# Kernel tuning notes

Hardware: AMD Instinct MI355X
Metric: run time of the kernel (lower is better)

The kernel has to match this reference:

```python
import jax, jax.numpy as jnp
import numpy as np

N_NODES = 50000
N_EDGES = 800000
IN_C, HID_C, OUT_C = 128, 128, 1


def setup_inputs() -> dict:
    key = jax.random.key(0)
    ks = jax.random.split(key, 10)
    x = jax.random.normal(ks[0], (N_NODES, IN_C), dtype=jnp.float32)
    x2 = jax.random.normal(ks[1], (1,), dtype=jnp.float32)
    edge_index = jax.random.randint(ks[2], (2, N_EDGES), 0, N_NODES, dtype=jnp.int64)
    # GCNConv params (glorot-ish scale) and final linear
    W1 = jax.random.normal(ks[3], (IN_C, HID_C), dtype=jnp.float32) / np.sqrt(IN_C)
    b1 = jnp.zeros((HID_C,), dtype=jnp.float32)
    W2 = jax.random.normal(ks[4], (HID_C, HID_C), dtype=jnp.float32) / np.sqrt(HID_C)
    b2 = jnp.zeros((HID_C,), dtype=jnp.float32)
    Wlin = jax.random.normal(ks[5], (HID_C, OUT_C), dtype=jnp.float32) / np.sqrt(HID_C)
    blin = jnp.zeros((OUT_C,), dtype=jnp.float32)
    return {"x": x, "x2": x2, "edge_index": edge_index, "num_nodes": N_NODES,
            "W1": W1, "b1": b1, "W2": W2, "b2": b2, "Wlin": Wlin, "blin": blin}


def _gcn_conv(h, W, b, src, dst, norm, num_nodes):
    # linear transform then normalized scatter-add aggregation (PyG GCNConv)
    h = h @ W  # [N, C_out]
    msg = h[src] * norm[:, None]  # gather + scale, [E+N, C_out]
    out = jax.ops.segment_sum(msg, dst, num_segments=num_nodes)
    return out + b


def _gcn_norm(edge_index, num_nodes):
    # add self-loops, compute sym-normalization coefficients D^-1/2 A D^-1/2
    loop = jnp.arange(num_nodes, dtype=edge_index.dtype)
    src = jnp.concatenate([edge_index[0], loop])
    dst = jnp.concatenate([edge_index[1], loop])
    ones = jnp.ones(src.shape[0], dtype=jnp.float32)
    deg = jax.ops.segment_sum(ones, dst, num_segments=num_nodes)
    dinv = jnp.where(deg > 0, jax.lax.rsqrt(deg), 0.0)
    norm = dinv[src] * dinv[dst]
    return src, dst, norm


def reference(x, x2, edge_index, num_nodes, W1, b1, W2, b2, Wlin, blin):
    src, dst, norm = _gcn_norm(edge_index, num_nodes)
    h = _gcn_conv(x, W1, b1, src, dst, norm, num_nodes)
    h = jax.nn.relu(h)
    # dropout is identity in eval mode
    h = _gcn_conv(h, W2, b2, src, dst, norm, num_nodes)
    h = jax.nn.relu(h)
    out = h @ Wlin + blin  # [N, 1]
    return out.squeeze(-1)
```

## Files before the change

### kernel.cpp

```cpp
#include <hip/hip_runtime.h>
#include <hip/hip_bf16.h>

#define N_NODES 50000
#define N_EDGES 800000
#define C 128

#define NBB   391
#define CAPB  2600
#define CHUNK 2048

typedef __attribute__((ext_vector_type(8))) short short8v;
typedef __attribute__((ext_vector_type(4))) float f32x4;

__device__ __forceinline__ unsigned int bf16rtn(float f) {
    unsigned int u = __float_as_uint(f);
    return (u + 0x7fffu + ((u >> 16) & 1u)) >> 16;
}
__device__ __forceinline__ unsigned int packbf2(float lo, float hi) {
    return bf16rtn(lo) | (bf16rtn(hi) << 16);
}

__global__ void k_prepW(const float* __restrict__ W1, const float* __restrict__ W2,
                        unsigned short* __restrict__ Wsplit, int* __restrict__ gcur) {
    int t = blockIdx.x * 256 + threadIdx.x;
    if (t < NBB) gcur[t] = 0;
    if (t >= 32768) return;
    int layer = t >> 14, idx = t & 16383;
    int i = idx >> 7, j = idx & 127;
    const float* Wsrc = layer ? W2 : W1;
    float w = Wsrc[i * 128 + j];
    unsigned int h = bf16rtn(w);
    float hf = __uint_as_float(h << 16);
    unsigned int l = bf16rtn(w - hf);
    unsigned short* base = Wsplit + layer * 32768;
    base[j * 128 + i] = (unsigned short)h;
    base[16384 + j * 128 + i] = (unsigned short)l;
}

__global__ __launch_bounds__(256) void k_binA(const int* __restrict__ ei,
                                              int* __restrict__ gcur,
                                              int2* __restrict__ tmp) {
    __shared__ int hist[NBB];
    __shared__ int lbase[NBB];
    __shared__ int gbaseL[NBB];
    __shared__ int wsum[4];
    __shared__ int2 buf[CHUNK];
    __shared__ int totalv;

    int tid = threadIdx.x;
    int e0 = blockIdx.x * CHUNK;

    for (int i = tid; i < NBB; i += 256) hist[i] = 0;
    __syncthreads();

    int sarr[8], darr[8], parr[8];
#pragma unroll
    for (int j = 0; j < 8; ++j) {
        int e = e0 + j * 256 + tid;
        darr[j] = -1;
        if (e < N_EDGES) {
            sarr[j] = ei[e];
            int d = ei[N_EDGES + e];
            darr[j] = d;
            parr[j] = atomicAdd(&hist[d >> 7], 1);
        }
    }
    __syncthreads();

    {
        int i0 = 2 * tid, i1 = i0 + 1;
        int c0 = (i0 < NBB) ? hist[i0] : 0;
        int c1 = (i1 < NBB) ? hist[i1] : 0;
        int c = c0 + c1;
        int lane = tid & 63, w = tid >> 6;
        int s = c;
#pragma unroll
        for (int d = 1; d < 64; d <<= 1) {
            int u = __shfl_up(s, d, 64);
            if (lane >= d) s += u;
        }
        if (lane == 63) wsum[w] = s;
        __syncthreads();
        int add = 0;
        for (int i = 0; i < w; ++i) add += wsum[i];
        int incl = s + add;
        int excl = incl - c;
        if (i0 < NBB) lbase[i0] = excl;
        if (i1 < NBB) lbase[i1] = excl + c0;
        if (tid == 255) totalv = incl;
    }
    for (int i = tid; i < NBB; i += 256) {
        int cnt = hist[i];
        int run = (cnt > 0) ? atomicAdd(&gcur[i], cnt) : 0;
        gbaseL[i] = i * CAPB + run;
    }
    __syncthreads();

#pragma unroll
    for (int j = 0; j < 8; ++j) {
        if (darr[j] >= 0) {
            int b = darr[j] >> 7;
            buf[lbase[b] + parr[j]] = make_int2(sarr[j], darr[j]);
        }
    }
    __syncthreads();

    int total = totalv;
    for (int i = tid; i < total; i += 256) {
        int2 v = buf[i];
        int b = v.y >> 7;
        int gpos = gbaseL[b] + (i - lbase[b]);
        if (gpos < (b + 1) * CAPB) tmp[gpos] = v;
    }
}

__global__ __launch_bounds__(256) void k_dinv(const int2* __restrict__ tmp,
                                              const int* __restrict__ gcur,
                                              float* __restrict__ dinv) {
    __shared__ int cnt[128];
    int b = blockIdx.x, tid = threadIdx.x;
    if (tid < 128) cnt[tid] = 0;
    __syncthreads();
    int n = gcur[b];
    if (n > CAPB) n = CAPB;
    for (int i = tid; i < n; i += 256)
        atomicAdd(&cnt[tmp[b * CAPB + i].y & 127], 1);
    __syncthreads();
    int node = b * 128 + tid;
    if (tid < 128 && node < N_NODES)
        dinv[node] = rsqrtf((float)cnt[tid] + 1.0f);
}

template <bool AF32>
__global__ __launch_bounds__(512, 4) void k_gemm(const void* __restrict__ Ain,
                                                 const unsigned short* __restrict__ Whg,
                                                 const unsigned short* __restrict__ Wlg,
                                                 const float* __restrict__ dinv,
                                                 unsigned short* __restrict__ Hout) {
    __shared__ uint4 Al[64 * 16];
    __shared__ float ddv[64];

    int tid = threadIdx.x;
    int row0 = blockIdx.x * 64;
    int wv = tid >> 6, lane = tid & 63;
    int col = wv * 16 + (lane & 15);
    int kq = lane >> 4;

    const uint4* Bh4 = (const uint4*)Whg;
    const uint4* Bl4 = (const uint4*)Wlg;
    short8v bh[4], bl[4];
#pragma unroll
    for (int ks = 0; ks < 4; ++ks) {
        uint4 uh = Bh4[col * 16 + ks * 4 + kq];
        uint4 ul = Bl4[col * 16 + ks * 4 + kq];
        bh[ks] = *reinterpret_cast<short8v*>(&uh);
        bl[ks] = *reinterpret_cast<short8v*>(&ul);
    }

#pragma unroll
    for (int pass = 0; pass < 2; ++pass) {
        int row = (tid >> 4) + pass * 32;
        int o = tid & 15;
        int gr = row0 + row;
        uint4 u = make_uint4(0u, 0u, 0u, 0u);
        if (AF32) {
            float4 v0 = make_float4(0.f, 0.f, 0.f, 0.f), v1 = v0;
            if (gr < N_NODES) {
                const float4* A4 = (const float4*)Ain;
                v0 = A4[gr * 32 + o * 2];
                v1 = A4[gr * 32 + o * 2 + 1];
            }
            u.x = packbf2(v0.x, v0.y);
            u.y = packbf2(v0.z, v0.w);
            u.z = packbf2(v1.x, v1.y);
            u.w = packbf2(v1.z, v1.w);
        } else {
            if (gr < N_NODES) u = ((const uint4*)Ain)[gr * 16 + o];
        }
        int byte = (row * 256 + o * 16) ^ ((row & 7) << 4);
        Al[byte >> 4] = u;
    }
    if (tid < 64) {
        int gr = row0 + tid;
        ddv[tid] = (gr < N_NODES) ? dinv[gr] : 0.f;
    }
    __syncthreads();

    f32x4 acc[4];
#pragma unroll
    for (int st = 0; st < 4; ++st) acc[st] = (f32x4){0.f, 0.f, 0.f, 0.f};

#pragma unroll
    for (int st = 0; st < 4; ++st) {
        int rowl = st * 16 + (lane & 15);
        int rbase = rowl * 256;
        int swz = (rowl & 7) << 4;
#pragma unroll
        for (int ks = 0; ks < 4; ++ks) {
            int byte = (rbase + ks * 64 + kq * 16) ^ swz;
            uint4 ua = Al[byte >> 4];
            short8v a = *reinterpret_cast<short8v*>(&ua);
            acc[st] = __builtin_amdgcn_mfma_f32_16x16x32_bf16(a, bh[ks], acc[st], 0, 0, 0);
            acc[st] = __builtin_amdgcn_mfma_f32_16x16x32_bf16(a, bl[ks], acc[st], 0, 0, 0);
        }
    }

#pragma unroll
    for (int st = 0; st < 4; ++st) {
#pragma unroll
        for (int r = 0; r < 4; ++r) {
            int rowl = st * 16 + kq * 4 + r;
            int gr = row0 + rowl;
            if (gr < N_NODES) {
                float dv = ddv[rowl];
                Hout[gr * 128 + col] = (unsigned short)bf16rtn(dv * acc[st][r]);
            }
        }
    }
}

__device__ __forceinline__ void add8(float* acc, uint4 u) {
    acc[0] += __uint_as_float(u.x << 16);
    acc[1] += __uint_as_float(u.x & 0xffff0000u);
    acc[2] += __uint_as_float(u.y << 16);
    acc[3] += __uint_as_float(u.y & 0xffff0000u);
    acc[4] += __uint_as_float(u.z << 16);
    acc[5] += __uint_as_float(u.z & 0xffff0000u);
    acc[6] += __uint_as_float(u.w << 16);
    acc[7] += __uint_as_float(u.w & 0xffff0000u);
}

template <bool FINAL>
__global__ __launch_bounds__(512, 6) void k_agg(const uint4* __restrict__ h4,
                                                const int2* __restrict__ tmp,
                                                const int* __restrict__ gcur,
                                                const float* __restrict__ bias,
                                                const float* __restrict__ Wlin,
                                                const float* __restrict__ blin,
                                                void* __restrict__ aggout) {
    __shared__ int   rawsrc[CAPB];
    __shared__ short rawloc[CAPB];
    __shared__ int   lcsr[CAPB];
    __shared__ int   lcnt[64];
    __shared__ int   lbase0[64];
    __shared__ int   lcur[64];

    int blk = blockIdx.x;
    int b = blk >> 1, half = blk & 1;
    int tid = threadIdx.x;
    int cnt = gcur[b];
    if (cnt > CAPB) cnt = CAPB;

    if (tid < 64) { lcnt[tid] = 0; lcur[tid] = 0; }
    __syncthreads();

    const int2* tmpb = tmp + (size_t)b * CAPB;
    for (int i = tid; i < cnt; i += 512) {
        int2 v = tmpb[i];
        int l = v.y & 127;
        rawsrc[i] = v.x;
        rawloc[i] = (short)l;
        if ((l >> 6) == half) atomicAdd(&lcnt[l & 63], 1);
    }
    __syncthreads();

    if (tid < 64) {
        int c = lcnt[tid];
        int s = c;
#pragma unroll
        for (int d = 1; d < 64; d <<= 1) {
            int u = __shfl_up(s, d, 64);
            if (tid >= d) s += u;
        }
        lbase0[tid] = s - c;
    }
    __syncthreads();

    for (int i = tid; i < cnt; i += 512) {
        int l = rawloc[i];
        if ((l >> 6) == half) {
            int ll = l & 63;
            int p = atomicAdd(&lcur[ll], 1);
            lcsr[lbase0[ll] + p] = rawsrc[i];
        }
    }
    __syncthreads();

    int wv = tid >> 6, lane = tid & 63, eg = lane >> 4, cq = lane & 15;

    float4 bv0 = ((const float4*)bias)[cq * 2];
    float4 bv1 = ((const float4*)bias)[cq * 2 + 1];
    float4 wl0 = make_float4(0.f, 0.f, 0.f, 0.f), wl1 = wl0;
    float bl = 0.f;
    if (FINAL) {
        wl0 = ((const float4*)Wlin)[cq * 2];
        wl1 = ((const float4*)Wlin)[cq * 2 + 1];
        bl = blin[0];
    }

#pragma unroll 1
    for (int t = 0; t < 8; ++t) {
        int ll = wv * 8 + t;
        int node = b * 128 + half * 64 + ll;
        if (node >= N_NODES) break;
        int deg = lcnt[ll];
        int o0 = lbase0[ll], o1 = o0 + deg;

        uint4 us = h4[node * 16 + cq];

        float acc[8];
#pragma unroll
        for (int j = 0; j < 8; ++j) acc[j] = 0.f;

        int e = o0;
        for (; e + 16 <= o1; e += 16) {
            int b0 = e + 4 * eg;
            int s0 = lcsr[b0], s1 = lcsr[b0 + 1], s2 = lcsr[b0 + 2], s3 = lcsr[b0 + 3];
            uint4 u0 = h4[s0 * 16 + cq];
            uint4 u1 = h4[s1 * 16 + cq];
            uint4 u2 = h4[s2 * 16 + cq];
            uint4 u3 = h4[s3 * 16 + cq];
            add8(acc, u0); add8(acc, u1); add8(acc, u2); add8(acc, u3);
        }
        if (e + 8 <= o1) {
            int b0 = e + 2 * eg;
            int s0 = lcsr[b0], s1 = lcsr[b0 + 1];
            uint4 u0 = h4[s0 * 16 + cq];
            uint4 u1 = h4[s1 * 16 + cq];
            add8(acc, u0); add8(acc, u1);
            e += 8;
        }
        {
            int r = o1 - e;
            int b0 = e + 2 * eg;
            if (2 * eg < r)     add8(acc, h4[lcsr[b0] * 16 + cq]);
            if (2 * eg + 1 < r) add8(acc, h4[lcsr[b0 + 1] * 16 + cq]);
        }
#pragma unroll
        for (int j = 0; j < 8; ++j) {
            acc[j] += __shfl_xor(acc[j], 16, 64);
            acc[j] += __shfl_xor(acc[j], 32, 64);
        }

        float dv = rsqrtf((float)deg + 1.0f);
        float hv[8];
        hv[0] = __uint_as_float(us.x << 16); hv[1] = __uint_as_float(us.x & 0xffff0000u);
        hv[2] = __uint_as_float(us.y << 16); hv[3] = __uint_as_float(us.y & 0xffff0000u);
        hv[4] = __uint_as_float(us.z << 16); hv[5] = __uint_as_float(us.z & 0xffff0000u);
        hv[6] = __uint_as_float(us.w << 16); hv[7] = __uint_as_float(us.w & 0xffff0000u);
        float o[8];
        o[0] = dv * (acc[0] + hv[0]) + bv0.x;
        o[1] = dv * (acc[1] + hv[1]) + bv0.y;
        o[2] = dv * (acc[2] + hv[2]) + bv0.z;
        o[3] = dv * (acc[3] + hv[3]) + bv0.w;
        o[4] = dv * (acc[4] + hv[4]) + bv1.x;
        o[5] = dv * (acc[5] + hv[5]) + bv1.y;
        o[6] = dv * (acc[6] + hv[6]) + bv1.z;
        o[7] = dv * (acc[7] + hv[7]) + bv1.w;

        if (!FINAL) {
            if (eg == 0) {
                uint4 u;
                u.x = packbf2(fmaxf(o[0], 0.f), fmaxf(o[1], 0.f));
                u.y = packbf2(fmaxf(o[2], 0.f), fmaxf(o[3], 0.f));
                u.z = packbf2(fmaxf(o[4], 0.f), fmaxf(o[5], 0.f));
                u.w = packbf2(fmaxf(o[6], 0.f), fmaxf(o[7], 0.f));
                ((uint4*)aggout)[node * 16 + cq] = u;
            }
        } else {
            float v = fmaxf(o[0], 0.f) * wl0.x + fmaxf(o[1], 0.f) * wl0.y
                    + fmaxf(o[2], 0.f) * wl0.z + fmaxf(o[3], 0.f) * wl0.w
                    + fmaxf(o[4], 0.f) * wl1.x + fmaxf(o[5], 0.f) * wl1.y
                    + fmaxf(o[6], 0.f) * wl1.z + fmaxf(o[7], 0.f) * wl1.w;
            v += __shfl_xor(v, 1, 64);
            v += __shfl_xor(v, 2, 64);
            v += __shfl_xor(v, 4, 64);
            v += __shfl_xor(v, 8, 64);
            if (lane == 0) ((float*)aggout)[node] = v + bl;
        }
    }
}

extern "C" void kernel_launch(void* const* d_in, const int* in_sizes, int n_in,
                              void* d_out, int out_size, void* d_ws, size_t ws_size,
                              hipStream_t stream) {
    const float* x    = (const float*)d_in[0];
    const int*   ei   = (const int*)d_in[2];
    const float* W1   = (const float*)d_in[4];
    const float* b1   = (const float*)d_in[5];
    const float* W2   = (const float*)d_in[6];
    const float* b2   = (const float*)d_in[7];
    const float* Wlin = (const float*)d_in[8];
    const float* blin = (const float*)d_in[9];
    float* out = (float*)d_out;

    char* ws = (char*)d_ws;
    size_t off = 0;
    auto carve = [&](size_t bytes) -> void* {
        void* p = ws + off;
        off = (off + bytes + 255) & ~(size_t)255;
        return p;
    };
    int*   gcur = (int*)  carve(NBB * sizeof(int));
    float* dinv = (float*)carve(N_NODES * sizeof(float));
    int2*  tmp  = (int2*) carve((size_t)NBB * CAPB * sizeof(int2));
    unsigned short* hbf  = (unsigned short*)carve((size_t)N_NODES * C * sizeof(unsigned short));
    unsigned short* hbf2 = (unsigned short*)carve((size_t)N_NODES * C * sizeof(unsigned short));
    unsigned short* wsplit = (unsigned short*)carve(4 * 16384 * sizeof(unsigned short));

    const int NB_A = (N_EDGES + CHUNK - 1) / CHUNK;
    const int NB_G = (N_NODES + 63) / 64;
    const int NB_H = 2 * NBB;

    const unsigned short* W1h = wsplit;
    const unsigned short* W1l = wsplit + 16384;
    const unsigned short* W2h = wsplit + 32768;
    const unsigned short* W2l = wsplit + 49152;

    k_prepW<<<128, 256, 0, stream>>>(W1, W2, wsplit, gcur);
    k_binA<<<NB_A, 256, 0, stream>>>(ei, gcur, tmp);
    k_dinv<<<NBB, 256, 0, stream>>>(tmp, gcur, dinv);

    k_gemm<true><<<NB_G, 512, 0, stream>>>(x, W1h, W1l, dinv, hbf);
    k_agg<false><<<NB_H, 512, 0, stream>>>((const uint4*)hbf, tmp, gcur,
                                           b1, Wlin, blin, hbf2);
    k_gemm<false><<<NB_G, 512, 0, stream>>>(hbf2, W2h, W2l, dinv, hbf);
    k_agg<true><<<NB_H, 512, 0, stream>>>((const uint4*)hbf, tmp, gcur,
                                          b2, Wlin, blin, out);
}
```

Baseline: 217.9 us.

## Build global padded CSR once and aggregate with one wave per node

The per-bucket CSR construction moves out of both aggregation kernels into a single k_csr pass. That pass writes a global 4-padded CSR along with per-node offset and degree arrays, replacing the old degree-only kernel. Aggregation then runs one wave per node with vectorized int4/int2 index loads and no shared-memory staging or barriers, which allows many more blocks. The costs are an extra global CSR buffer and global index reads in place of LDS reads. CAPB also grows from 2600 to 3072, which lowers the chance of silently dropping edges in buckets that overflow.

Measured after the change: 202.8 us. -6.9%, faster.

```diff
diff --git a/kernel.cpp b/kernel.cpp
--- a/kernel.cpp
+++ b/kernel.cpp
@@ -6,7 +6,8 @@
 #define C 128
 
 #define NBB   391
-#define CAPB  2600
+#define CAPB  3072
+#define CAPC  3456
 #define CHUNK 2048
 
 typedef __attribute__((ext_vector_type(8))) short short8v;
@@ -114,21 +115,63 @@
     }
 }
 
-__global__ __launch_bounds__(256) void k_dinv(const int2* __restrict__ tmp,
-                                              const int* __restrict__ gcur,
-                                              float* __restrict__ dinv) {
-    __shared__ int cnt[128];
+__global__ __launch_bounds__(256) void k_csr(const int2* __restrict__ tmp,
+                                             const int* __restrict__ gcur,
+                                             int* __restrict__ csr,
+                                             int* __restrict__ offn,
+                                             int* __restrict__ degn,
+                                             float* __restrict__ dinv) {
+    __shared__ int   rawsrc[CAPB];
+    __shared__ short rawloc[CAPB];
+    __shared__ int   lcnt[128];
+    __shared__ int   lbase[128];
+    __shared__ int   lcur[128];
+
     int b = blockIdx.x, tid = threadIdx.x;
-    if (tid < 128) cnt[tid] = 0;
-    __syncthreads();
-    int n = gcur[b];
-    if (n > CAPB) n = CAPB;
-    for (int i = tid; i < n; i += 256)
-        atomicAdd(&cnt[tmp[b * CAPB + i].y & 127], 1);
-    __syncthreads();
+    int cnt = gcur[b];
+    if (cnt > CAPB) cnt = CAPB;
+
+    if (tid < 128) { lcnt[tid] = 0; lcur[tid] = 0; }
+    __syncthreads();
+
+    const int2* tmpb = tmp + (size_t)b * CAPB;
+    for (int i = tid; i < cnt; i += 256) {
+        int2 v = tmpb[i];
+        int l = v.y & 127;
+        rawsrc[i] = v.x;
+        rawloc[i] = (short)l;
+        atomicAdd(&lcnt[l], 1);
+    }
+    __syncthreads();
+
+    if (tid < 64) {
+        int c0 = lcnt[2 * tid], c1 = lcnt[2 * tid + 1];
+        int p0 = (c0 + 3) & ~3, p1 = (c1 + 3) & ~3;
+        int c = p0 + p1;
+        int s = c;
+#pragma unroll
+        for (int d = 1; d < 64; d <<= 1) {
+            int u = __shfl_up(s, d, 64);
+            if (tid >= d) s += u;
+        }
+        int excl = s - c;
+        lbase[2 * tid] = excl;
+        lbase[2 * tid + 1] = excl + p0;
+    }
+    __syncthreads();
+
     int node = b * 128 + tid;
-    if (tid < 128 && node < N_NODES)
-        dinv[node] = rsqrtf((float)cnt[tid] + 1.0f);
+    if (tid < 128 && node < N_NODES) {
+        offn[node] = b * CAPC + lbase[tid];
+        degn[node] = lcnt[tid];
+        dinv[node] = rsqrtf((float)lcnt[tid] + 1.0f);
+    }
+
+    for (int i = tid; i < cnt; i += 256) {
+        int l = rawloc[i];
+        int p = atomicAdd(&lcur[l], 1);
+        csr[b * CAPC + lbase[l] + p] = rawsrc[i];
+    }
 }
 
 template <bool AF32>
@@ -231,153 +274,94 @@
 }
 
 template <bool FINAL>
-__global__ __launch_bounds__(512, 6) void k_agg(const uint4* __restrict__ h4,
-                                                const int2* __restrict__ tmp,
-                                                const int* __restrict__ gcur,
-                                                const float* __restrict__ bias,
-                                                const float* __restrict__ Wlin,
-                                                const float* __restrict__ blin,
-                                                void* __restrict__ aggout) {
-    __shared__ int   rawsrc[CAPB];
-    __shared__ short rawloc[CAPB];
-    __shared__ int   lcsr[CAPB];
-    __shared__ int   lcnt[64];
-    __shared__ int   lbase0[64];
-    __shared__ int   lcur[64];
-
-    int blk = blockIdx.x;
-    int b = blk >> 1, half = blk & 1;
-    int tid = threadIdx.x;
-    int cnt = gcur[b];
-    if (cnt > CAPB) cnt = CAPB;
-
-    if (tid < 64) { lcnt[tid] = 0; lcur[tid] = 0; }
-    __syncthreads();
-
-    const int2* tmpb = tmp + (size_t)b * CAPB;
-    for (int i = tid; i < cnt; i += 512) {
-        int2 v = tmpb[i];
-        int l = v.y & 127;
-        rawsrc[i] = v.x;
-        rawloc[i] = (short)l;
-        if ((l >> 6) == half) atomicAdd(&lcnt[l & 63], 1);
-    }
-    __syncthreads();
-
-    if (tid < 64) {
-        int c = lcnt[tid];
-        int s = c;
-#pragma unroll
-        for (int d = 1; d < 64; d <<= 1) {
-            int u = __shfl_up(s, d, 64);
-            if (tid >= d) s += u;
-        }
-        lbase0[tid] = s - c;
-    }
-    __syncthreads();
-
-    for (int i = tid; i < cnt; i += 512) {
-        int l = rawloc[i];
-        if ((l >> 6) == half) {
-            int ll = l & 63;
-            int p = atomicAdd(&lcur[ll], 1);
-            lcsr[lbase0[ll] + p] = rawsrc[i];
-        }
-    }
-    __syncthreads();
-
-    int wv = tid >> 6, lane = tid & 63, eg = lane >> 4, cq = lane & 15;
-
+__global__ __launch_bounds__(256) void k_agg(const uint4* __restrict__ h4,
+                                             const int* __restrict__ csr,
+                                             const int* __restrict__ offn,
+                                             const int* __restrict__ degn,
+                                             const float* __restrict__ bias,
+                                             const float* __restrict__ Wlin,
+                                             const float* __restrict__ blin,
+                                             void* __restrict__ aggout) {
+    int n = (blockIdx.x * 256 + threadIdx.x) >> 6;
+    int lane = threadIdx.x & 63, eg = lane >> 4, cq = lane & 15;
+
+    int o0 = offn[n];
+    int deg = degn[n];
+    int end = o0 + deg;
+
+    uint4 us = h4[n * 16 + cq];
+
+    float acc[8];
+#pragma unroll
+    for (int j = 0; j < 8; ++j) acc[j] = 0.f;
+
+    int e = o0;
+    for (; e + 16 <= end; e += 16) {
+        int4 s4 = *(const int4*)(csr + e + 4 * eg);
+        uint4 u0 = h4[s4.x * 16 + cq];
+        uint4 u1 = h4[s4.y * 16 + cq];
+        uint4 u2 = h4[s4.z * 16 + cq];
+        uint4 u3 = h4[s4.w * 16 + cq];
+        add8(acc, u0); add8(acc, u1); add8(acc, u2); add8(acc, u3);
+    }
+    if (e + 8 <= end) {
+        int2 s2 = *(const int2*)(csr + e + 2 * eg);
+        uint4 u0 = h4[s2.x * 16 + cq];
+        uint4 u1 = h4[s2.y * 16 + cq];
+        add8(acc, u0); add8(acc, u1);
+        e += 8;
+    }
+    {
+        int r = end - e;
+        int b0 = e + 2 * eg;
+        if (2 * eg < r)     add8(acc, h4[csr[b0] * 16 + cq]);
+        if (2 * eg + 1 < r) add8(acc, h4[csr[b0 + 1] * 16 + cq]);
+    }
+#pragma unroll
+    for (int j = 0; j < 8; ++j) {
+        acc[j] += __shfl_xor(acc[j], 16, 64);
+        acc[j] += __shfl_xor(acc[j], 32, 64);
+    }
+
+    float dv = rsqrtf((float)deg + 1.0f);
     float4 bv0 = ((const float4*)bias)[cq * 2];
     float4 bv1 = ((const float4*)bias)[cq * 2 + 1];
-    float4 wl0 = make_float4(0.f, 0.f, 0.f, 0.f), wl1 = wl0;
-    float bl = 0.f;
-    if (FINAL) {
-        wl0 = ((const float4*)Wlin)[cq * 2];
-        wl1 = ((const float4*)Wlin)[cq * 2 + 1];
-        bl = blin[0];
-    }
-
-#pragma unroll 1
-    for (int t = 0; t < 8; ++t) {
-        int ll = wv * 8 + t;
-        int node = b * 128 + half * 64 + ll;
-        if (node >= N_NODES) break;
-        int deg = lcnt[ll];
-        int o0 = lbase0[ll], o1 = o0 + deg;
-
-        uint4 us = h4[node * 16 + cq];
-
-        float acc[8];
-#pragma unroll
-        for (int j = 0; j < 8; ++j) acc[j] = 0.f;
-
-        int e = o0;
-        for (; e + 16 <= o1; e += 16) {
-            int b0 = e + 4 * eg;
-            int s0 = lcsr[b0], s1 = lcsr[b0 + 1], s2 = lcsr[b0 + 2], s3 = lcsr[b0 + 3];
-            uint4 u0 = h4[s0 * 16 + cq];
-            uint4 u1 = h4[s1 * 16 + cq];
-            uint4 u2 = h4[s2 * 16 + cq];
-            uint4 u3 = h4[s3 * 16 + cq];
-            add8(acc, u0); add8(acc, u1); add8(acc, u2); add8(acc, u3);
-        }
-        if (e + 8 <= o1) {
-            int b0 = e + 2 * eg;
-            int s0 = lcsr[b0], s1 = lcsr[b0 + 1];
-            uint4 u0 = h4[s0 * 16 + cq];
-            uint4 u1 = h4[s1 * 16 + cq];
-            add8(acc, u0); add8(acc, u1);
-            e += 8;
-        }
-        {
-            int r = o1 - e;
-            int b0 = e + 2 * eg;
-            if (2 * eg < r)     add8(acc, h4[lcsr[b0] * 16 + cq]);
-            if (2 * eg + 1 < r) add8(acc, h4[lcsr[b0 + 1] * 16 + cq]);
-        }
-#pragma unroll
-        for (int j = 0; j < 8; ++j) {
-            acc[j] += __shfl_xor(acc[j], 16, 64);
-            acc[j] += __shfl_xor(acc[j], 32, 64);
-        }
-
-        float dv = rsqrtf((float)deg + 1.0f);
-        float hv[8];
-        hv[0] = __uint_as_float(us.x << 16); hv[1] = __uint_as_float(us.x & 0xffff0000u);
-        hv[2] = __uint_as_float(us.y << 16); hv[3] = __uint_as_float(us.y & 0xffff0000u);
-        hv[4] = __uint_as_float(us.z << 16); hv[5] = __uint_as_float(us.z & 0xffff0000u);
-        hv[6] = __uint_as_float(us.w << 16); hv[7] = __uint_as_float(us.w & 0xffff0000u);
-        float o[8];
-        o[0] = dv * (acc[0] + hv[0]) + bv0.x;
-        o[1] = dv * (acc[1] + hv[1]) + bv0.y;
-        o[2] = dv * (acc[2] + hv[2]) + bv0.z;
-        o[3] = dv * (acc[3] + hv[3]) + bv0.w;
-        o[4] = dv * (acc[4] + hv[4]) + bv1.x;
-        o[5] = dv * (acc[5] + hv[5]) + bv1.y;
-        o[6] = dv * (acc[6] + hv[6]) + bv1.z;
-        o[7] = dv * (acc[7] + hv[7]) + bv1.w;
-
-        if (!FINAL) {
-            if (eg == 0) {
-                uint4 u;
-                u.x = packbf2(fmaxf(o[0], 0.f), fmaxf(o[1], 0.f));
-                u.y = packbf2(fmaxf(o[2], 0.f), fmaxf(o[3], 0.f));
-                u.z = packbf2(fmaxf(o[4], 0.f), fmaxf(o[5], 0.f));
-                u.w = packbf2(fmaxf(o[6], 0.f), fmaxf(o[7], 0.f));
-                ((uint4*)aggout)[node * 16 + cq] = u;
-            }
-        } else {
-            float v = fmaxf(o[0], 0.f) * wl0.x + fmaxf(o[1], 0.f) * wl0.y
-                    + fmaxf(o[2], 0.f) * wl0.z + fmaxf(o[3], 0.f) * wl0.w
-                    + fmaxf(o[4], 0.f) * wl1.x + fmaxf(o[5], 0.f) * wl1.y
-                    + fmaxf(o[6], 0.f) * wl1.z + fmaxf(o[7], 0.f) * wl1.w;
-            v += __shfl_xor(v, 1, 64);
-            v += __shfl_xor(v, 2, 64);
-            v += __shfl_xor(v, 4, 64);
-            v += __shfl_xor(v, 8, 64);
-            if (lane == 0) ((float*)aggout)[node] = v + bl;
-        }
+    float hv[8];
+    hv[0] = __uint_as_float(us.x << 16); hv[1] = __uint_as_float(us.x & 0xffff0000u);
+    hv[2] = __uint_as_float(us.y << 16); hv[3] = __uint_as_float(us.y & 0xffff0000u);
+    hv[4] = __uint_as_float(us.z << 16); hv[5] = __uint_as_float(us.z & 0xffff0000u);
+    hv[6] = __uint_as_float(us.w << 16); hv[7] = __uint_as_float(us.w & 0xffff0000u);
+    float o[8];
+    o[0] = dv * (acc[0] + hv[0]) + bv0.x;
+    o[1] = dv * (acc[1] + hv[1]) + bv0.y;
+    o[2] = dv * (acc[2] + hv[2]) + bv0.z;
+    o[3] = dv * (acc[3] + hv[3]) + bv0.w;
+    o[4] = dv * (acc[4] + hv[4]) + bv1.x;
+    o[5] = dv * (acc[5] + hv[5]) + bv1.y;
+    o[6] = dv * (acc[6] + hv[6]) + bv1.z;
+    o[7] = dv * (acc[7] + hv[7]) + bv1.w;
+
+    if (!FINAL) {
+        if (eg == 0) {
+            uint4 u;
+            u.x = packbf2(fmaxf(o[0], 0.f), fmaxf(o[1], 0.f));
+            u.y = packbf2(fmaxf(o[2], 0.f), fmaxf(o[3], 0.f));
+            u.z = packbf2(fmaxf(o[4], 0.f), fmaxf(o[5], 0.f));
+            u.w = packbf2(fmaxf(o[6], 0.f), fmaxf(o[7], 0.f));
+            ((uint4*)aggout)[n * 16 + cq] = u;
+        }
+    } else {
+        float4 wl0 = ((const float4*)Wlin)[cq * 2];
+        float4 wl1 = ((const float4*)Wlin)[cq * 2 + 1];
+        float v = fmaxf(o[0], 0.f) * wl0.x + fmaxf(o[1], 0.f) * wl0.y
+                + fmaxf(o[2], 0.f) * wl0.z + fmaxf(o[3], 0.f) * wl0.w
+                + fmaxf(o[4], 0.f) * wl1.x + fmaxf(o[5], 0.f) * wl1.y
+                + fmaxf(o[6], 0.f) * wl1.z + fmaxf(o[7], 0.f) * wl1.w;
+        v += __shfl_xor(v, 1, 64);
+        v += __shfl_xor(v, 2, 64);
+        v += __shfl_xor(v, 4, 64);
+        v += __shfl_xor(v, 8, 64);
+        if (lane == 0) ((float*)aggout)[n] = v + blin[0];
     }
 }
 
@@ -403,14 +387,17 @@
     };
     int*   gcur = (int*)  carve(NBB * sizeof(int));
     float* dinv = (float*)carve(N_NODES * sizeof(float));
+    int*   offn = (int*)  carve(N_NODES * sizeof(int));
+    int*   degn = (int*)  carve(N_NODES * sizeof(int));
     int2*  tmp  = (int2*) carve((size_t)NBB * CAPB * sizeof(int2));
+    int*   csr  = (int*)  carve((size_t)NBB * CAPC * sizeof(int));
     unsigned short* hbf  = (unsigned short*)carve((size_t)N_NODES * C * sizeof(unsigned short));
     unsigned short* hbf2 = (unsigned short*)carve((size_t)N_NODES * C * sizeof(unsigned short));
     unsigned short* wsplit = (unsigned short*)carve(4 * 16384 * sizeof(unsigned short));
 
     const int NB_A = (N_EDGES + CHUNK - 1) / CHUNK;
     const int NB_G = (N_NODES + 63) / 64;
-    const int NB_H = 2 * NBB;
+    const int NB_W = (N_NODES * 64) / 256;
 
     const unsigned short* W1h = wsplit;
     const unsigned short* W1l = wsplit + 16384;
@@ -419,12 +406,12 @@
 
     k_prepW<<<128, 256, 0, stream>>>(W1, W2, wsplit, gcur);
     k_binA<<<NB_A, 256, 0, stream>>>(ei, gcur, tmp);
-    k_dinv<<<NBB, 256, 0, stream>>>(tmp, gcur, dinv);
+    k_csr<<<NBB, 256, 0, stream>>>(tmp, gcur, csr, offn, degn, dinv);
 
     k_gemm<true><<<NB_G, 512, 0, stream>>>(x, W1h, W1l, dinv, hbf);
-    k_agg<false><<<NB_H, 512, 0, stream>>>((const uint4*)hbf, tmp, gcur,
+    k_agg<false><<<NB_W, 256, 0, stream>>>((const uint4*)hbf, csr, offn, degn,
                                            b1, Wlin, blin, hbf2);
     k_gemm<false><<<NB_G, 512, 0, stream>>>(hbf2, W2h, W2l, dinv, hbf);
-    k_agg<true><<<NB_H, 512, 0, stream>>>((const uint4*)hbf, tmp, gcur,
+    k_agg<true><<<NB_W, 256, 0, stream>>>((const uint4*)hbf, csr, offn, degn,
                                           b2, Wlin, blin, out);
 }
```
